# Kernel tuning notes

Measured on AMD Instinct MI355X. Metric: run time of the kernel, lower is better.

Reference implementation:

```python
import jax, jax.numpy as jnp
import numpy as np

B, N, NPOINT, NSAMPLE = 8, 16384, 512, 64
RADIUS = 0.1
C_IN = 64
DIMS = [64, 64, 128]


def setup_inputs() -> dict:
    key = jax.random.key(0)
    ks = jax.random.split(key, 8)
    xyz = jax.random.uniform(ks[0], (B, N, 3), jnp.float32)          # points in unit cube
    features = jax.random.normal(ks[1], (B, C_IN, N), jnp.float32)   # (B, C, N) per GroupGatherByIndex
    dims = [3 + C_IN] + DIMS                                         # use_xyz_feature adds 3
    out = {"xyz": xyz, "features": features}
    for i in range(3):
        out[f"W{i+1}"] = jax.random.normal(ks[2 + i], (dims[i], dims[i + 1]), jnp.float32) / np.sqrt(dims[i])
        out[f"b{i+1}"] = jnp.zeros((dims[i + 1],), jnp.float32)
    return out


def furthest_point_sampling(xyz, npoint):
    # Iterative FPS starting at index 0 (matches CUDA kernel semantics).
    Bq, Nq, _ = xyz.shape
    barange = jnp.arange(Bq)

    def step(carry, _):
        dists, last = carry
        p = xyz[barange, last]                       # (B, 3)
        d = jnp.sum((xyz - p[:, None, :]) ** 2, -1)  # (B, N)
        dists = jnp.minimum(dists, d)
        nxt = jnp.argmax(dists, axis=1).astype(jnp.int32)
        return (dists, nxt), nxt

    init = (jnp.full((Bq, Nq), 1e10, xyz.dtype), jnp.zeros((Bq,), jnp.int32))
    _, idxs = jax.lax.scan(step, init, None, length=npoint - 1)
    return jnp.concatenate([jnp.zeros((Bq, 1), jnp.int32), idxs.T], axis=1)  # (B, npoint)


def ball_query(new_xyz, xyz, radius, nsample):
    # For each centroid, first nsample in-ball indices (ascending), padded with first hit.
    Nq = xyz.shape[1]
    d2 = jnp.sum((new_xyz[:, :, None, :] - xyz[:, None, :, :]) ** 2, -1)  # (B, npoint, N)
    cand = jnp.where(d2 < radius * radius, jnp.arange(Nq, dtype=jnp.int32), Nq)
    cand = jnp.sort(cand, axis=-1)[..., :nsample]                          # (B, npoint, nsample)
    first = jnp.where(cand[..., :1] == Nq, 0, cand[..., :1])
    return jnp.where(cand == Nq, first, cand)


def reference(xyz, features, W1, b1, W2, b2, W3, b3):
    fps_idx = furthest_point_sampling(xyz, NPOINT)                  # (B, npoint)
    new_xyz = jax.vmap(lambda p, i: p[i])(xyz, fps_idx)             # (B, npoint, 3)
    idx = ball_query(new_xyz, xyz, RADIUS, NSAMPLE)                 # (B, npoint, nsample)
    grouped_xyz = jax.vmap(lambda p, i: p[i])(xyz, idx)             # (B, npoint, nsample, 3)
    centered = grouped_xyz - new_xyz[:, :, None, :]                 # centroid subtract
    feats_n = jnp.transpose(features, (0, 2, 1))                    # (B, N, C)
    grouped_f = jax.vmap(lambda f, i: f[i])(feats_n, idx)           # (B, npoint, nsample, C)
    h = jnp.concatenate([centered, grouped_f], axis=-1)             # (B, npoint, nsample, 3+C)
    for W, b in ((W1, b1), (W2, b2), (W3, b3)):                     # pointwise 1x1-conv MLP + ReLU
        h = jax.nn.relu(h @ W + b)
    return jnp.max(h, axis=2)                                       # max-pool over nsample -> (B, npoint, C_out)
```

## Files before the change

kernel.cpp:

```cpp
#include <hip/hip_runtime.h>

#define NB 8
#define NPTS 16384
#define NPOINT 512
#define NSAMPLE 64
#define CIN 64

typedef float v2f __attribute__((ext_vector_type(2)));

template <int CTRL>
__device__ __forceinline__ float dpp_f(float x) {
    int xi = __builtin_bit_cast(int, x);
    int yi = __builtin_amdgcn_update_dpp(xi, xi, CTRL, 0xF, 0xF, false);
    return __builtin_bit_cast(float, yi);
}
template <int CTRL>
__device__ __forceinline__ int dpp_i(int x) {
    return __builtin_amdgcn_update_dpp(x, x, CTRL, 0xF, 0xF, false);
}

__device__ __forceinline__ float wave_max_f(float x) {
    x = fmaxf(x, dpp_f<0x111>(x));
    x = fmaxf(x, dpp_f<0x112>(x));
    x = fmaxf(x, dpp_f<0x114>(x));
    x = fmaxf(x, dpp_f<0x118>(x));
    x = fmaxf(x, dpp_f<0x142>(x));
    x = fmaxf(x, dpp_f<0x143>(x));
    return x;
}
__device__ __forceinline__ int wave_min_i(int x) {
    x = min(x, dpp_i<0x111>(x));
    x = min(x, dpp_i<0x112>(x));
    x = min(x, dpp_i<0x114>(x));
    x = min(x, dpp_i<0x118>(x));
    x = min(x, dpp_i<0x142>(x));
    x = min(x, dpp_i<0x143>(x));
    return x;
}

#define CMB(va, ia, vb, ib) { bool t_ = ((vb) > (va)) || (((vb) == (va)) && ((ib) < (ia))); \
                              if (t_) { (va) = (vb); (ia) = (ib); } }

__global__ __launch_bounds__(512) __attribute__((amdgpu_waves_per_eu(2, 2)))
void fps_transpose_kernel(
    const float* __restrict__ xyz, const float* __restrict__ feats,
    int* __restrict__ fps_idx, float* __restrict__ feats_t)
{
    __shared__ float t[64][65];
    __shared__ __align__(16) int s_pair[2][8][2];

    if (blockIdx.x >= NB) {
        int blk = blockIdx.x - NB;
        int b = blk & 7;
        int tile = blk >> 3;
        int n0 = tile * 64;
        int cc = threadIdx.x & 63, rr = threadIdx.x >> 6;
        const float* fb = feats + (size_t)b * CIN * NPTS;
        #pragma unroll
        for (int k = 0; k < 8; ++k) {
            int c = rr + k * 8;
            t[c][cc] = fb[(size_t)c * NPTS + n0 + cc];
        }
        __syncthreads();
        float* fo = feats_t + ((size_t)b * NPTS + n0) * CIN;
        #pragma unroll
        for (int k = 0; k < 8; ++k) {
            int n = rr + k * 8;
            fo[n * CIN + cc] = t[cc][n];
        }
        return;
    }

    __builtin_amdgcn_s_setprio(1);
    const int b = blockIdx.x;
    const int tid = threadIdx.x;
    const int wv = tid >> 6, ln = tid & 63;
    const float* xb = xyz + (size_t)b * NPTS * 3;
    const int base = tid * 32;

    v2f px2[16], py2[16], pz2[16], dd2[16];
    {
        const float4* xb4 = (const float4*)(xb + (size_t)base * 3);
        #pragma unroll
        for (int q = 0; q < 8; ++q) {
            float4 f0 = xb4[3 * q + 0];
            float4 f1 = xb4[3 * q + 1];
            float4 f2 = xb4[3 * q + 2];
            px2[2 * q + 0] = (v2f){f0.x, f0.w};
            py2[2 * q + 0] = (v2f){f0.y, f1.x};
            pz2[2 * q + 0] = (v2f){f0.z, f1.y};
            px2[2 * q + 1] = (v2f){f1.z, f2.y};
            py2[2 * q + 1] = (v2f){f1.w, f2.z};
            pz2[2 * q + 1] = (v2f){f2.x, f2.w};
        }
        #pragma unroll
        for (int k = 0; k < 16; ++k) dd2[k] = (v2f){1e10f, 1e10f};
    }
    if (tid == 0) fps_idx[b * NPOINT] = 0;
    float cx = xb[0], cy = xb[1], cz = xb[2];
    __syncthreads();

    for (int j = 1; j < NPOINT; ++j) {
        #pragma clang fp contract(off)
        const int p = j & 1;
        v2f ncx = (v2f){-cx, -cx};
        v2f ncy = (v2f){-cy, -cy};
        v2f ncz = (v2f){-cz, -cz};
        float bm = -1.0f;
        #pragma unroll
        for (int k = 0; k < 16; ++k) {
            v2f dx = px2[k] + ncx;
            v2f dy = py2[k] + ncy;
            v2f dz = pz2[k] + ncz;
            v2f s1 = dx * dx + dy * dy;
            v2f d2 = s1 + dz * dz;
            v2f nd = __builtin_elementwise_min(dd2[k], d2);
            dd2[k] = nd;
            bm = fmaxf(bm, fmaxf(nd.x, nd.y));
        }
        float wm = wave_max_f(bm);
        float wmax = __builtin_bit_cast(float,
            __builtin_amdgcn_readlane(__builtin_bit_cast(int, wm), 63));
        int mk = 64;
        #pragma unroll
        for (int k = 15; k >= 0; --k) {
            mk = (dd2[k].y == wmax) ? (2 * k + 1) : mk;
            mk = (dd2[k].x == wmax) ? (2 * k)     : mk;
        }
        int mi = (mk == 64) ? 0x7fffffff : (base + mk);
        int rm = wave_min_i(mi);
        int wave_mi = __builtin_amdgcn_readlane(rm, 63);
        if (ln == 0) {
            s_pair[p][wv][0] = __builtin_bit_cast(int, wmax);
            s_pair[p][wv][1] = wave_mi;
        }
        __syncthreads();
        int4 q0 = *(const int4*)&s_pair[p][0][0];
        int4 q1 = *(const int4*)&s_pair[p][2][0];
        int4 q2 = *(const int4*)&s_pair[p][4][0];
        int4 q3 = *(const int4*)&s_pair[p][6][0];
        float v0 = __builtin_bit_cast(float, q0.x); int i0 = q0.y;
        float v1 = __builtin_bit_cast(float, q0.z); int i1 = q0.w;
        float v2 = __builtin_bit_cast(float, q1.x); int i2 = q1.y;
        float v3 = __builtin_bit_cast(float, q1.z); int i3 = q1.w;
        float v4 = __builtin_bit_cast(float, q2.x); int i4 = q2.y;
        float v5 = __builtin_bit_cast(float, q2.z); int i5 = q2.w;
        float v6 = __builtin_bit_cast(float, q3.x); int i6 = q3.y;
        float v7 = __builtin_bit_cast(float, q3.z); int i7 = q3.w;
        CMB(v0, i0, v1, i1); CMB(v2, i2, v3, i3);
        CMB(v4, i4, v5, i5); CMB(v6, i6, v7, i7);
        CMB(v0, i0, v2, i2); CMB(v4, i4, v6, i6);
        CMB(v0, i0, v4, i4);
        int ch = __builtin_amdgcn_readfirstlane(i0);
        const float* cp = xb + 3 * ch;
        cx = cp[0]; cy = cp[1]; cz = cp[2];
        if (tid == 0) fps_idx[b * NPOINT + j] = ch;
    }
}

__global__ __launch_bounds__(64) void ballmlp_kernel(
    const float* __restrict__ xyz, const float* __restrict__ feats_t,
    const int* __restrict__ fps_idx,
    const float* __restrict__ W1, const float* __restrict__ b1,
    const float* __restrict__ W2, const float* __restrict__ b2,
    const float* __restrict__ W3, const float* __restrict__ b3,
    float* __restrict__ out)
{
    const float R2 = (float)(0.1 * 0.1);
    int blk = blockIdx.x;
    int b = blk & 7, j = blk >> 3;
    int s = threadIdx.x;
    int cent = b * NPOINT + j;
    const float* xb = xyz + (size_t)b * NPTS * 3;

    __shared__ float X[67][64];
    __shared__ int slots[64];

    int cidx = fps_idx[cent];
    float cx = xb[3 * cidx + 0];
    float cy = xb[3 * cidx + 1];
    float cz = xb[3 * cidx + 2];

    int cnt = 0;
    for (int bs = 0; bs < NPTS; bs += 64) {
        int i = bs + s;
        float dx = __fsub_rn(xb[3 * i + 0], cx);
        float dy = __fsub_rn(xb[3 * i + 1], cy);
        float dz = __fsub_rn(xb[3 * i + 2], cz);
        float d2 = __fadd_rn(__fadd_rn(__fmul_rn(dx, dx), __fmul_rn(dy, dy)), __fmul_rn(dz, dz));
        bool inb = d2 < R2;
        unsigned long long m = __ballot(inb);
        int pre = (int)__popcll(m & ((1ull << s) - 1ull));
        int slot = cnt + pre;
        if (inb && slot < NSAMPLE) slots[slot] = i;
        cnt += (int)__popcll(m);
        if (cnt >= NSAMPLE) break;
    }
    __syncthreads();
    int first = (cnt > 0) ? slots[0] : 0;
    int i = (s < cnt) ? slots[s] : first;

    const float* pp = xyz + ((size_t)b * NPTS + i) * 3;
    X[64][s] = pp[0] - cx;
    X[65][s] = pp[1] - cy;
    X[66][s] = pp[2] - cz;
    const float4* fr = (const float4*)(feats_t + ((size_t)b * NPTS + i) * CIN);
    #pragma unroll
    for (int q = 0; q < 16; ++q) {
        float4 f = fr[q];
        X[q * 4 + 0][s] = f.x;
        X[q * 4 + 1][s] = f.y;
        X[q * 4 + 2][s] = f.z;
        X[q * 4 + 3][s] = f.w;
    }

    float acc[64];
    #pragma unroll
    for (int o = 0; o < 64; ++o) acc[o] = b1[o];
    for (int c = 0; c < 67; ++c) {
        float xc = X[c][s];
        const float* w = W1 + ((c < 64) ? (c + 3) : (c - 64)) * 64;
        #pragma unroll
        for (int o = 0; o < 64; ++o) acc[o] = fmaf(xc, w[o], acc[o]);
    }
    #pragma unroll
    for (int o = 0; o < 64; ++o) X[o][s] = fmaxf(acc[o], 0.0f);

    #pragma unroll
    for (int o = 0; o < 64; ++o) acc[o] = b2[o];
    for (int c = 0; c < 64; ++c) {
        float xc = X[c][s];
        const float* w = W2 + c * 64;
        #pragma unroll
        for (int o = 0; o < 64; ++o) acc[o] = fmaf(xc, w[o], acc[o]);
    }
    #pragma unroll
    for (int o = 0; o < 64; ++o) X[o][s] = fmaxf(acc[o], 0.0f);

    float h3[128];
    #pragma unroll
    for (int o = 0; o < 128; ++o) h3[o] = b3[o];
    for (int c = 0; c < 64; ++c) {
        float xc = X[c][s];
        const float* w = W3 + c * 128;
        #pragma unroll
        for (int o = 0; o < 128; ++o) h3[o] = fmaf(xc, w[o], h3[o]);
    }

    #pragma unroll
    for (int o = 0; o < 128; ++o) {
        float v = fmaxf(h3[o], 0.0f);
        #pragma unroll
        for (int off = 1; off < 64; off <<= 1) v = fmaxf(v, __shfl_xor(v, off));
        h3[o] = v;
    }
    if (s == 0) {
        float* op = out + (size_t)cent * 128;
        #pragma unroll
        for (int o = 0; o < 128; o += 4) {
            float4 v = make_float4(h3[o], h3[o + 1], h3[o + 2], h3[o + 3]);
            *(float4*)&op[o] = v;
        }
    }
}

extern "C" void kernel_launch(void* const* d_in, const int* in_sizes, int n_in,
                              void* d_out, int out_size, void* d_ws, size_t ws_size,
                              hipStream_t stream) {
    const float* xyz   = (const float*)d_in[0];
    const float* feats = (const float*)d_in[1];
    const float* W1 = (const float*)d_in[2];
    const float* b1 = (const float*)d_in[3];
    const float* W2 = (const float*)d_in[4];
    const float* b2 = (const float*)d_in[5];
    const float* W3 = (const float*)d_in[6];
    const float* b3 = (const float*)d_in[7];
    float* out = (float*)d_out;

    char* ws = (char*)d_ws;
    int*   fps_idx  = (int*)ws;
    float* feats_t  = (float*)(ws + 65536);

    fps_transpose_kernel<<<NB + NB * (NPTS / 64), 512, 0, stream>>>(xyz, feats, fps_idx, feats_t);
    ballmlp_kernel<<<NB * NPOINT, 64, 0, stream>>>(xyz, feats_t, fps_idx,
                                                   W1, b1, W2, b2, W3, b3, out);
}
```

Baseline: 1.212 ms.

## Widen FPS blocks to 1024 threads and use DPP cross-wave argmax

```diff
diff --git a/kernel.cpp b/kernel.cpp
--- a/kernel.cpp
+++ b/kernel.cpp
@@ -5,6 +5,7 @@
 #define NPOINT 512
 #define NSAMPLE 64
 #define CIN 64
+#define PPT 16
 
 typedef float v2f __attribute__((ext_vector_type(2)));
 
@@ -38,16 +39,13 @@
     return x;
 }
 
-#define CMB(va, ia, vb, ib) { bool t_ = ((vb) > (va)) || (((vb) == (va)) && ((ib) < (ia))); \
-                              if (t_) { (va) = (vb); (ia) = (ib); } }
-
-__global__ __launch_bounds__(512) __attribute__((amdgpu_waves_per_eu(2, 2)))
+__global__ __launch_bounds__(1024) __attribute__((amdgpu_waves_per_eu(4)))
 void fps_transpose_kernel(
     const float* __restrict__ xyz, const float* __restrict__ feats,
     int* __restrict__ fps_idx, float* __restrict__ feats_t)
 {
     __shared__ float t[64][65];
-    __shared__ __align__(16) int s_pair[2][8][2];
+    __shared__ __align__(16) int s_pair[2][16][2];
 
     if (blockIdx.x >= NB) {
         int blk = blockIdx.x - NB;
@@ -57,32 +55,31 @@
         int cc = threadIdx.x & 63, rr = threadIdx.x >> 6;
         const float* fb = feats + (size_t)b * CIN * NPTS;
         #pragma unroll
-        for (int k = 0; k < 8; ++k) {
-            int c = rr + k * 8;
+        for (int k = 0; k < 4; ++k) {
+            int c = rr + k * 16;
             t[c][cc] = fb[(size_t)c * NPTS + n0 + cc];
         }
         __syncthreads();
         float* fo = feats_t + ((size_t)b * NPTS + n0) * CIN;
         #pragma unroll
-        for (int k = 0; k < 8; ++k) {
-            int n = rr + k * 8;
+        for (int k = 0; k < 4; ++k) {
+            int n = rr + k * 16;
             fo[n * CIN + cc] = t[cc][n];
         }
         return;
     }
 
-    __builtin_amdgcn_s_setprio(1);
     const int b = blockIdx.x;
     const int tid = threadIdx.x;
     const int wv = tid >> 6, ln = tid & 63;
     const float* xb = xyz + (size_t)b * NPTS * 3;
-    const int base = tid * 32;
-
-    v2f px2[16], py2[16], pz2[16], dd2[16];
+    const int base = tid * PPT;
+
+    v2f px2[8], py2[8], pz2[8], dd2[8];
     {
         const float4* xb4 = (const float4*)(xb + (size_t)base * 3);
         #pragma unroll
-        for (int q = 0; q < 8; ++q) {
+        for (int q = 0; q < 4; ++q) {
             float4 f0 = xb4[3 * q + 0];
             float4 f1 = xb4[3 * q + 1];
             float4 f2 = xb4[3 * q + 2];
@@ -94,7 +91,7 @@
             pz2[2 * q + 1] = (v2f){f2.x, f2.w};
         }
         #pragma unroll
-        for (int k = 0; k < 16; ++k) dd2[k] = (v2f){1e10f, 1e10f};
+        for (int k = 0; k < 8; ++k) dd2[k] = (v2f){1e10f, 1e10f};
     }
     if (tid == 0) fps_idx[b * NPOINT] = 0;
     float cx = xb[0], cy = xb[1], cz = xb[2];
@@ -108,7 +105,7 @@
         v2f ncz = (v2f){-cz, -cz};
         float bm = -1.0f;
         #pragma unroll
-        for (int k = 0; k < 16; ++k) {
+        for (int k = 0; k < 8; ++k) {
             v2f dx = px2[k] + ncx;
             v2f dy = py2[k] + ncy;
             v2f dz = pz2[k] + ncz;
@@ -123,9 +120,10 @@
             __builtin_amdgcn_readlane(__builtin_bit_cast(int, wm), 63));
         int mk = 64;
         #pragma unroll
-        for (int k = 15; k >= 0; --k) {
-            mk = (dd2[k].y == wmax) ? (2 * k + 1) : mk;
-            mk = (dd2[k].x == wmax) ? (2 * k)     : mk;
+        for (int k = 0; k < 8; ++k) {
+            int ca = (dd2[k].x == wmax) ? (2 * k)     : 64;
+            int cb = (dd2[k].y == wmax) ? (2 * k + 1) : 64;
+            mk = min(mk, min(ca, cb));
         }
         int mi = (mk == 64) ? 0x7fffffff : (base + mk);
         int rm = wave_min_i(mi);
@@ -135,23 +133,21 @@
             s_pair[p][wv][1] = wave_mi;
         }
         __syncthreads();
-        int4 q0 = *(const int4*)&s_pair[p][0][0];
-        int4 q1 = *(const int4*)&s_pair[p][2][0];
-        int4 q2 = *(const int4*)&s_pair[p][4][0];
-        int4 q3 = *(const int4*)&s_pair[p][6][0];
-        float v0 = __builtin_bit_cast(float, q0.x); int i0 = q0.y;
-        float v1 = __builtin_bit_cast(float, q0.z); int i1 = q0.w;
-        float v2 = __builtin_bit_cast(float, q1.x); int i2 = q1.y;
-        float v3 = __builtin_bit_cast(float, q1.z); int i3 = q1.w;
-        float v4 = __builtin_bit_cast(float, q2.x); int i4 = q2.y;
-        float v5 = __builtin_bit_cast(float, q2.z); int i5 = q2.w;
-        float v6 = __builtin_bit_cast(float, q3.x); int i6 = q3.y;
-        float v7 = __builtin_bit_cast(float, q3.z); int i7 = q3.w;
-        CMB(v0, i0, v1, i1); CMB(v2, i2, v3, i3);
-        CMB(v4, i4, v5, i5); CMB(v6, i6, v7, i7);
-        CMB(v0, i0, v2, i2); CMB(v4, i4, v6, i6);
-        CMB(v0, i0, v4, i4);
-        int ch = __builtin_amdgcn_readfirstlane(i0);
+        int2 pr = *(const int2*)&s_pair[p][ln & 15][0];
+        float v = __builtin_bit_cast(float, pr.x);
+        int   i = pr.y;
+        {
+            float ov; int oi; bool tk;
+            ov = dpp_f<0x111>(v); oi = dpp_i<0x111>(i);
+            tk = (ov > v) || (ov == v && oi < i); v = tk ? ov : v; i = tk ? oi : i;
+            ov = dpp_f<0x112>(v); oi = dpp_i<0x112>(i);
+            tk = (ov > v) || (ov == v && oi < i); v = tk ? ov : v; i = tk ? oi : i;
+            ov = dpp_f<0x114>(v); oi = dpp_i<0x114>(i);
+            tk = (ov > v) || (ov == v && oi < i); v = tk ? ov : v; i = tk ? oi : i;
+            ov = dpp_f<0x118>(v); oi = dpp_i<0x118>(i);
+            tk = (ov > v) || (ov == v && oi < i); v = tk ? ov : v; i = tk ? oi : i;
+        }
+        int ch = __builtin_amdgcn_readlane(i, 15);
         const float* cp = xb + 3 * ch;
         cx = cp[0]; cy = cp[1]; cz = cp[2];
         if (tid == 0) fps_idx[b * NPOINT + j] = ch;
@@ -248,13 +244,9 @@
     }
 
     #pragma unroll
-    for (int o = 0; o < 128; ++o) {
-        float v = fmaxf(h3[o], 0.0f);
-        #pragma unroll
-        for (int off = 1; off < 64; off <<= 1) v = fmaxf(v, __shfl_xor(v, off));
-        h3[o] = v;
-    }
-    if (s == 0) {
+    for (int o = 0; o < 128; ++o)
+        h3[o] = wave_max_f(fmaxf(h3[o], 0.0f));
+    if (s == 63) {
         float* op = out + (size_t)cent * 128;
         #pragma unroll
         for (int o = 0; o < 128; o += 4) {
@@ -281,7 +273,7 @@
     int*   fps_idx  = (int*)ws;
     float* feats_t  = (float*)(ws + 65536);
 
-    fps_transpose_kernel<<<NB + NB * (NPTS / 64), 512, 0, stream>>>(xyz, feats, fps_idx, feats_t);
+    fps_transpose_kernel<<<NB + NB * (NPTS / 64), 1024, 0, stream>>>(xyz, feats, fps_idx, feats_t);
     ballmlp_kernel<<<NB * NPOINT, 64, 0, stream>>>(xyz, feats_t, fps_idx,
                                                    W1, b1, W2, b2, W3, b3, out);
 }
```

New measurement: 1.241 ms. 1.02x slower.

## Split FPS per batch across four blocks with global atomic slot exchange

Applied to the files above, without the earlier changes.

```diff
diff --git a/kernel.cpp b/kernel.cpp
--- a/kernel.cpp
+++ b/kernel.cpp
@@ -5,8 +5,11 @@
 #define NPOINT 512
 #define NSAMPLE 64
 #define CIN 64
+#define PARTS 4
+#define PPB (NPTS / PARTS)
 
 typedef float v2f __attribute__((ext_vector_type(2)));
+typedef unsigned long long u64;
 
 template <int CTRL>
 __device__ __forceinline__ float dpp_f(float x) {
@@ -41,48 +44,45 @@
 #define CMB(va, ia, vb, ib) { bool t_ = ((vb) > (va)) || (((vb) == (va)) && ((ib) < (ia))); \
                               if (t_) { (va) = (vb); (ia) = (ib); } }
 
-__global__ __launch_bounds__(512) __attribute__((amdgpu_waves_per_eu(2, 2)))
-void fps_transpose_kernel(
-    const float* __restrict__ xyz, const float* __restrict__ feats,
-    int* __restrict__ fps_idx, float* __restrict__ feats_t)
+__global__ __launch_bounds__(256) void transpose_kernel(
+    const float* __restrict__ feats, float* __restrict__ feats_t)
 {
     __shared__ float t[64][65];
+    int blk = blockIdx.x;
+    int b = blk & 7, tile = blk >> 3, n0 = tile * 64;
+    int cc = threadIdx.x & 63, rr = threadIdx.x >> 6;
+    const float* fb = feats + (size_t)b * CIN * NPTS;
+    #pragma unroll
+    for (int k = 0; k < 16; ++k) {
+        int c = k * 4 + rr;
+        t[c][cc] = fb[(size_t)c * NPTS + n0 + cc];
+    }
+    __syncthreads();
+    float* fo = feats_t + ((size_t)b * NPTS + n0) * CIN;
+    #pragma unroll
+    for (int k = 0; k < 16; ++k) {
+        int n = k * 4 + rr;
+        fo[(size_t)n * CIN + cc] = t[cc][n];
+    }
+}
+
+__global__ __launch_bounds__(512) void fps_kernel(
+    const float* __restrict__ xyz, int* __restrict__ fps_idx, u64* __restrict__ slots)
+{
     __shared__ __align__(16) int s_pair[2][8][2];
 
-    if (blockIdx.x >= NB) {
-        int blk = blockIdx.x - NB;
-        int b = blk & 7;
-        int tile = blk >> 3;
-        int n0 = tile * 64;
-        int cc = threadIdx.x & 63, rr = threadIdx.x >> 6;
-        const float* fb = feats + (size_t)b * CIN * NPTS;
-        #pragma unroll
-        for (int k = 0; k < 8; ++k) {
-            int c = rr + k * 8;
-            t[c][cc] = fb[(size_t)c * NPTS + n0 + cc];
-        }
-        __syncthreads();
-        float* fo = feats_t + ((size_t)b * NPTS + n0) * CIN;
-        #pragma unroll
-        for (int k = 0; k < 8; ++k) {
-            int n = rr + k * 8;
-            fo[n * CIN + cc] = t[cc][n];
-        }
-        return;
-    }
-
-    __builtin_amdgcn_s_setprio(1);
-    const int b = blockIdx.x;
+    const int blk = blockIdx.x;
+    const int b = blk >> 2, part = blk & 3;
     const int tid = threadIdx.x;
     const int wv = tid >> 6, ln = tid & 63;
     const float* xb = xyz + (size_t)b * NPTS * 3;
-    const int base = tid * 32;
-
-    v2f px2[16], py2[16], pz2[16], dd2[16];
+    const int base = part * PPB + tid * 8;
+
+    v2f px2[4], py2[4], pz2[4], dd2[4];
     {
         const float4* xb4 = (const float4*)(xb + (size_t)base * 3);
         #pragma unroll
-        for (int q = 0; q < 8; ++q) {
+        for (int q = 0; q < 2; ++q) {
             float4 f0 = xb4[3 * q + 0];
             float4 f1 = xb4[3 * q + 1];
             float4 f2 = xb4[3 * q + 2];
@@ -94,11 +94,11 @@
             pz2[2 * q + 1] = (v2f){f2.x, f2.w};
         }
         #pragma unroll
-        for (int k = 0; k < 16; ++k) dd2[k] = (v2f){1e10f, 1e10f};
-    }
-    if (tid == 0) fps_idx[b * NPOINT] = 0;
+        for (int k = 0; k < 4; ++k) dd2[k] = (v2f){1e10f, 1e10f};
+    }
+    if (tid == 0 && part == 0) fps_idx[b * NPOINT] = 0;
     float cx = xb[0], cy = xb[1], cz = xb[2];
-    __syncthreads();
+    u64* myslots = slots + b * 8;
 
     for (int j = 1; j < NPOINT; ++j) {
         #pragma clang fp contract(off)
@@ -108,7 +108,7 @@
         v2f ncz = (v2f){-cz, -cz};
         float bm = -1.0f;
         #pragma unroll
-        for (int k = 0; k < 16; ++k) {
+        for (int k = 0; k < 4; ++k) {
             v2f dx = px2[k] + ncx;
             v2f dy = py2[k] + ncy;
             v2f dz = pz2[k] + ncz;
@@ -121,13 +121,13 @@
         float wm = wave_max_f(bm);
         float wmax = __builtin_bit_cast(float,
             __builtin_amdgcn_readlane(__builtin_bit_cast(int, wm), 63));
-        int mk = 64;
-        #pragma unroll
-        for (int k = 15; k >= 0; --k) {
+        int mk = 8;
+        #pragma unroll
+        for (int k = 3; k >= 0; --k) {
             mk = (dd2[k].y == wmax) ? (2 * k + 1) : mk;
             mk = (dd2[k].x == wmax) ? (2 * k)     : mk;
         }
-        int mi = (mk == 64) ? 0x7fffffff : (base + mk);
+        int mi = (mk == 8) ? 0x7fffffff : (base + mk);
         int rm = wave_min_i(mi);
         int wave_mi = __builtin_amdgcn_readlane(rm, 63);
         if (ln == 0) {
@@ -151,10 +151,28 @@
         CMB(v4, i4, v5, i5); CMB(v6, i6, v7, i7);
         CMB(v0, i0, v2, i2); CMB(v4, i4, v6, i6);
         CMB(v0, i0, v4, i4);
-        int ch = __builtin_amdgcn_readfirstlane(i0);
+        if (tid == 0) {
+            u64 msg = ((u64)(unsigned)__builtin_bit_cast(int, v0) << 32)
+                    | ((u64)(unsigned)j << 14) | (u64)(unsigned)i0;
+            __hip_atomic_store(&myslots[p * PARTS + part], msg,
+                               __ATOMIC_RELEASE, __HIP_MEMORY_SCOPE_AGENT);
+        }
+        float bv = -1.0f; int bi = 0x7fffffff;
+        #pragma unroll
+        for (int q = 0; q < PARTS; ++q) {
+            u64 t;
+            do {
+                t = __hip_atomic_load(&myslots[p * PARTS + q],
+                                      __ATOMIC_ACQUIRE, __HIP_MEMORY_SCOPE_AGENT);
+            } while ((unsigned)((t & 0xFFFFFFFFu) >> 14) != (unsigned)j);
+            float qv = __builtin_bit_cast(float, (int)(unsigned)(t >> 32));
+            int   qi = (int)(t & 0x3FFFu);
+            CMB(bv, bi, qv, qi);
+        }
+        int ch = __builtin_amdgcn_readfirstlane(bi);
         const float* cp = xb + 3 * ch;
         cx = cp[0]; cy = cp[1]; cz = cp[2];
-        if (tid == 0) fps_idx[b * NPOINT + j] = ch;
+        if (tid == 0 && part == 0) fps_idx[b * NPOINT + j] = ch;
     }
 }
 
@@ -248,13 +266,9 @@
     }
 
     #pragma unroll
-    for (int o = 0; o < 128; ++o) {
-        float v = fmaxf(h3[o], 0.0f);
-        #pragma unroll
-        for (int off = 1; off < 64; off <<= 1) v = fmaxf(v, __shfl_xor(v, off));
-        h3[o] = v;
-    }
-    if (s == 0) {
+    for (int o = 0; o < 128; ++o)
+        h3[o] = wave_max_f(fmaxf(h3[o], 0.0f));
+    if (s == 63) {
         float* op = out + (size_t)cent * 128;
         #pragma unroll
         for (int o = 0; o < 128; o += 4) {
@@ -278,10 +292,12 @@
     float* out = (float*)d_out;
 
     char* ws = (char*)d_ws;
-    int*   fps_idx  = (int*)ws;
-    float* feats_t  = (float*)(ws + 65536);
-
-    fps_transpose_kernel<<<NB + NB * (NPTS / 64), 512, 0, stream>>>(xyz, feats, fps_idx, feats_t);
+    int*   fps_idx = (int*)ws;
+    u64*   slots   = (u64*)(ws + 16384);
+    float* feats_t = (float*)(ws + 65536);
+
+    transpose_kernel<<<NB * (NPTS / 64), 256, 0, stream>>>(feats, feats_t);
+    fps_kernel<<<NB * PARTS, 512, 0, stream>>>(xyz, fps_idx, slots);
     ballmlp_kernel<<<NB * NPOINT, 64, 0, stream>>>(xyz, feats_t, fps_idx,
                                                    W1, b1, W2, b2, W3, b3, out);
 }
```

Result: slower. 4.578 ms (+277.9%).
